# Kernel tuning notes

Measured on AMD Instinct MI355X. Metric: run time of the kernel, lower is better.

The kernel has to match this reference:

```python
import jax, jax.numpy as jnp
import numpy as np

KH, KW, STRIDE = 3, 3, 1

def setup_inputs() -> dict:
    key = jax.random.key(0)
    x = jax.random.normal(key, (32, 64, 64, 64), dtype=jnp.float32)  # [B, C, H, W]
    return {"x": x}

def unfold(x, Kh, Kw, stride):
    B, C, H, W = x.shape
    Ho = H - (Kh - 1)  # number of row positions (loop bound in original)
    Wo = W - (Kw - 1)
    # Gather all patches with a small fixed Kh*Kw loop (vectorized over B,C,Ho,Wo).
    # Original flattens each patch [C, Kh, Kw] -> C*Kh*Kw (channel-major),
    # and enumerates positions row-major (i outer, j inner).
    slabs = [x[:, :, i * stride:i * stride + Ho, j * stride:j * stride + Wo]
             for i in range(Kh) for j in range(Kw)]          # each [B, C, Ho, Wo]
    p = jnp.stack(slabs, axis=2)                              # [B, C, Kh*Kw, Ho, Wo]
    return p.reshape(B, C * Kh * Kw, Ho * Wo)                 # [B, C*Kh*Kw, L]

def reference(x):
    return unfold(x, KH, KW, STRIDE)
```

## Files before the change

kernel.cpp:

```cpp
#include <hip/hip_runtime.h>


#define B 32
#define C 64
#define H 64
#define W 64
#define HO 62
#define WO 62
#define L (HO * WO)
#define L4 (L / 4)
#define KK 9

__device__ __forceinline__ int sw(int p) { return p + (p >> 5); }

__global__ __launch_bounds__(256) void unfold_kernel(
    const float* __restrict__ x, float* __restrict__ out) {
    __shared__ float tile[H * W + (H * W) / 32];

    const int c   = blockIdx.x;
    const int b   = blockIdx.y;
    const int tid = threadIdx.x;

    const float4* __restrict__ src =
        (const float4*)(x + (((size_t)(b * C + c)) << 12));
#pragma unroll
    for (int r = 0; r < 4; ++r) {
        const int p4 = tid + r * 256;
        float4 v = src[p4];
        const int p = p4 * 4;
        tile[sw(p)]     = v.x;
        tile[sw(p + 1)] = v.y;
        tile[sw(p + 2)] = v.z;
        tile[sw(p + 3)] = v.w;
    }
    __syncthreads();

    float4* __restrict__ dst =
        (float4*)out + (size_t)(b * C + c) * KK * L4;

#pragma unroll
    for (int k = 0; k < KK; ++k) {
        const int i = k / 3;
        const int j = k - i * 3;
        const int base = i * W + j;
        for (int t = tid; t < L4; t += 256) {
            const int l0 = t * 4;
            int ho = l0 / WO;
            int wo = l0 - ho * WO;
            int addr = base + ho * W + wo;
            float r[4];
#pragma unroll
            for (int q = 0; q < 4; ++q) {
                r[q] = tile[sw(addr)];
                ++addr;
                ++wo;
                if (wo == WO) { wo = 0; addr += (W - WO); }
            }
            float4 v;
            v.x = r[0]; v.y = r[1]; v.z = r[2]; v.w = r[3];
            dst[k * L4 + t] = v;
        }
    }
}

extern "C" void kernel_launch(void* const* d_in, const int* in_sizes, int n_in,
                              void* d_out, int out_size, void* d_ws, size_t ws_size,
                              hipStream_t stream) {
    const float* x = (const float*)d_in[0];
    float* out = (float*)d_out;

    dim3 block(256, 1, 1);
    dim3 grid(C, B, 1);
    unfold_kernel<<<grid, block, 0, stream>>>(x, out);
}
```

Baseline: 313.7 us.

## Replace LDS-staged unfold with direct row-wise global gather and scalar stores

Drops the shared-memory staging of each 64x64 channel plane and the float4 output packing. Each wavefront now handles output rows: lanes map to output columns, read the nine shifted inputs straight from global memory (relying on cache), and write scalar coalesced stores. This removes the LDS traffic, the barrier and the per-element index arithmetic, but it turns 16-byte stores into 4-byte stores, leaves 2 of 64 lanes idle, and adds redundant global loads.

```diff
diff --git a/kernel.cpp b/kernel.cpp
--- a/kernel.cpp
+++ b/kernel.cpp
@@ -8,57 +8,31 @@
 #define HO 62
 #define WO 62
 #define L (HO * WO)
-#define L4 (L / 4)
 #define KK 9
-
-__device__ __forceinline__ int sw(int p) { return p + (p >> 5); }
 
 __global__ __launch_bounds__(256) void unfold_kernel(
     const float* __restrict__ x, float* __restrict__ out) {
-    __shared__ float tile[H * W + (H * W) / 32];
+    const int c    = blockIdx.x;
+    const int b    = blockIdx.y;
+    const int tid  = threadIdx.x;
+    const int wid  = tid >> 6;
+    const int lane = tid & 63;
 
-    const int c   = blockIdx.x;
-    const int b   = blockIdx.y;
-    const int tid = threadIdx.x;
+    const float* __restrict__ xr = x + (((size_t)(b * C + c)) << 12);
+    float* __restrict__ o = out + (size_t)(b * C + c) * KK * L;
 
-    const float4* __restrict__ src =
-        (const float4*)(x + (((size_t)(b * C + c)) << 12));
+    if (lane < WO) {
+        for (int ho = wid; ho < HO; ho += 4) {
+            const float* __restrict__ row0 = xr + ho * W + lane;
+            float* __restrict__ orow = o + ho * WO + lane;
 #pragma unroll
-    for (int r = 0; r < 4; ++r) {
-        const int p4 = tid + r * 256;
-        float4 v = src[p4];
-        const int p = p4 * 4;
-        tile[sw(p)]     = v.x;
-        tile[sw(p + 1)] = v.y;
-        tile[sw(p + 2)] = v.z;
-        tile[sw(p + 3)] = v.w;
-    }
-    __syncthreads();
-
-    float4* __restrict__ dst =
-        (float4*)out + (size_t)(b * C + c) * KK * L4;
-
+            for (int i = 0; i < 3; ++i) {
+                const float* __restrict__ ri = row0 + i * W;
 #pragma unroll
-    for (int k = 0; k < KK; ++k) {
-        const int i = k / 3;
-        const int j = k - i * 3;
-        const int base = i * W + j;
-        for (int t = tid; t < L4; t += 256) {
-            const int l0 = t * 4;
-            int ho = l0 / WO;
-            int wo = l0 - ho * WO;
-            int addr = base + ho * W + wo;
-            float r[4];
-#pragma unroll
-            for (int q = 0; q < 4; ++q) {
-                r[q] = tile[sw(addr)];
-                ++addr;
-                ++wo;
-                if (wo == WO) { wo = 0; addr += (W - WO); }
+                for (int j = 0; j < 3; ++j) {
+                    orow[(i * 3 + j) * L] = ri[j];
+                }
             }
-            float4 v;
-            v.x = r[0]; v.y = r[1]; v.z = r[2]; v.w = r[3];
-            dst[k * L4 + t] = v;
         }
     }
 }
```

Measured after the change: 352.0 us. +12.2%, slower.
